# Kernel optimization log

Measured on AMD Instinct MI355X. Metric: run time of the kernel, lower is better.

The kernel has to match this reference:

```python
import jax, jax.numpy as jnp
import numpy as np

HIDDEN = 2048
N_HEADS = 16
N_KV = 8
HEAD_DIM = 128
EPS = 1e-6
THETA = 1000000.0
T = 2048


def _rmsnorm(x, w):
    # x: [T, h, D]; normalize over last dim
    var = jnp.mean(x * x, axis=-1, keepdims=True)
    return x * jax.lax.rsqrt(var + EPS) * w


def _rope(x, positions):
    # neox-style rotate-half, rotary_dim == head_dim
    D = x.shape[-1]
    inv_freq = 1.0 / (THETA ** (jnp.arange(0, D, 2, dtype=jnp.float32) / D))  # [D/2]
    freqs = positions.astype(jnp.float32)[:, None] * inv_freq  # [T, D/2]
    cos = jnp.cos(freqs)[:, None, :]  # [T, 1, D/2]
    sin = jnp.sin(freqs)[:, None, :]
    x1, x2 = jnp.split(x, 2, axis=-1)
    return jnp.concatenate([x1 * cos - x2 * sin, x2 * cos + x1 * sin], axis=-1)


def setup_inputs() -> dict:
    key = jax.random.key(0)
    ks = jax.random.split(key, 7)
    s = 0.02
    return {
        "positions": jnp.arange(T, dtype=jnp.int32),
        "hidden_states": jax.random.normal(ks[0], (T, HIDDEN), dtype=jnp.float32),
        "wq": jax.random.normal(ks[1], (HIDDEN, N_HEADS * HEAD_DIM), dtype=jnp.float32) * s,
        "wk": jax.random.normal(ks[2], (HIDDEN, N_KV * HEAD_DIM), dtype=jnp.float32) * s,
        "wv": jax.random.normal(ks[3], (HIDDEN, N_KV * HEAD_DIM), dtype=jnp.float32) * s,
        "wo": jax.random.normal(ks[4], (N_HEADS * HEAD_DIM, HIDDEN), dtype=jnp.float32) * s,
        "q_norm_w": jnp.ones((HEAD_DIM,), dtype=jnp.float32),
        "k_norm_w": jnp.ones((HEAD_DIM,), dtype=jnp.float32),
    }


def reference(positions, hidden_states, wq, wk, wv, wo, q_norm_w, k_norm_w):
    q = (hidden_states @ wq).reshape(-1, N_HEADS, HEAD_DIM)
    k = (hidden_states @ wk).reshape(-1, N_KV, HEAD_DIM)
    v = (hidden_states @ wv).reshape(-1, N_KV, HEAD_DIM)
    q = _rmsnorm(q, q_norm_w)
    k = _rmsnorm(k, k_norm_w)
    q = _rope(q, positions)
    k = _rope(k, positions)
    # GQA: expand kv heads
    rep = N_HEADS // N_KV
    k = jnp.repeat(k, rep, axis=1)  # [T, H, D]
    v = jnp.repeat(v, rep, axis=1)
    scale = HEAD_DIM ** -0.5
    scores = jnp.einsum('qhd,khd->hqk', q, k) * scale  # [H, T, T]
    tq = q.shape[0]
    causal = jnp.tril(jnp.ones((tq, tq), dtype=bool))
    scores = jnp.where(causal[None], scores, jnp.finfo(scores.dtype).min)
    probs = jax.nn.softmax(scores, axis=-1)
    o = jnp.einsum('hqk,khd->qhd', probs, v).reshape(tq, N_HEADS * HEAD_DIM)
    return o @ wo
```

## Files before the change

### kernel.cpp

```cpp
#include <hip/hip_runtime.h>
#include <cstdint>

#define TT 2048
#define NH 16
#define NKV 8
#define HD 128
#define SCALE_L2E 0.12751743f
#define SM_M2 16.5f

typedef unsigned short u16;
typedef unsigned int u32;
typedef u16 u16x8 __attribute__((ext_vector_type(8)));
typedef __bf16 bf16x8 __attribute__((ext_vector_type(8)));
typedef float f32x4 __attribute__((ext_vector_type(4)));

__device__ inline u16 f2bf(float x){
  u32 u = __builtin_bit_cast(u32, x);
  u = (u + 0x7fffu + ((u >> 16) & 1u)) >> 16;
  return (u16)u;
}
__device__ inline float bf2f(u16 h){
  return __builtin_bit_cast(float, (u32)h << 16);
}
__device__ inline bf16x8 as_bf(u16x8 v){ return __builtin_bit_cast(bf16x8, v); }

__device__ inline void gl_lds16(const void* g, void* l){
  typedef __attribute__((address_space(1))) const void gv_t;
  typedef __attribute__((address_space(3))) void lv_t;
  __builtin_amdgcn_global_load_lds((gv_t*)g, (lv_t*)l, 16, 0, 0);
}

__global__ void cast_f32_bf16(const float* __restrict__ in, u16* __restrict__ out, int n8){
  int i = blockIdx.x * blockDim.x + threadIdx.x;
  if (i < n8){
    const float4* p = (const float4*)(in + (size_t)i * 8);
    float4 a = p[0], b = p[1];
    u16x8 o = { f2bf(a.x), f2bf(a.y), f2bf(a.z), f2bf(a.w),
                f2bf(b.x), f2bf(b.y), f2bf(b.z), f2bf(b.w) };
    *(u16x8*)(out + (size_t)i * 8) = o;
  }
}

__global__ void transpose_cast(const float* __restrict__ in, u16* __restrict__ out, int R, int C){
  __shared__ float tile[32][33];
  int bx = blockIdx.x * 32;
  int by = blockIdx.y * 32;
  int x = threadIdx.x, y = threadIdx.y;
  #pragma unroll
  for (int i = 0; i < 32; i += 8) tile[y + i][x] = in[(size_t)(by + y + i) * C + bx + x];
  __syncthreads();
  #pragma unroll
  for (int i = 0; i < 32; i += 8) out[(size_t)(bx + y + i) * R + by + x] = f2bf(tile[x][y + i]);
}

template<bool F32OUT>
__global__ __launch_bounds__(256, 2) void gemm_bt(const u16* __restrict__ A, const u16* __restrict__ B,
                                                  void* __restrict__ C, int K,
                                                  int lda, int ldb, int ldc){
  __shared__ u16 lds[2][(128 + 128) * 64];
  const int tid = threadIdx.x;
  const int wv = tid >> 6, ln = tid & 63;
  const int lg = ln >> 4, l15 = ln & 15;
  const int m0 = blockIdx.y * 128, n0 = blockIdx.x * 128;
  const int wr = wv >> 1, wc = wv & 1;
  f32x4 acc[4][4] = {};

  auto stage = [&](int buf, int kt){
    const u16* Ab = A + (size_t)m0 * lda + kt * 64;
    const u16* Bb = B + (size_t)n0 * ldb + kt * 64;
    u16* lA = &lds[buf][0];
    u16* lB = &lds[buf][128 * 64];
    #pragma unroll
    for (int it = 0; it < 4; ++it){
      int idx = it * 256 + tid;
      int r = idx >> 3, cs = idx & 7;
      gl_lds16(Ab + (size_t)r * lda + cs * 8, lA + (size_t)(it * 256 + wv * 64) * 8);
    }
    #pragma unroll
    for (int it = 0; it < 4; ++it){
      int idx = it * 256 + tid;
      int r = idx >> 3, cs = idx & 7;
      gl_lds16(Bb + (size_t)r * ldb + cs * 8, lB + (size_t)(it * 256 + wv * 64) * 8);
    }
  };

  stage(0, 0);
  int nk = K / 64;
  for (int kt = 0; kt < nk; ++kt){
    int buf = kt & 1;
    __syncthreads();
    if (kt + 1 < nk) stage(buf ^ 1, kt + 1);
    const u16* lA = &lds[buf][0];
    const u16* lB = &lds[buf][128 * 64];
    #pragma unroll
    for (int kk = 0; kk < 2; ++kk){
      int kof = kk * 32 + lg * 8;
      bf16x8 af[4], bfv[4];
      #pragma unroll
      for (int mm = 0; mm < 4; mm++){
        int row = wr * 64 + mm * 16 + l15;
        af[mm] = as_bf(*(const u16x8*)&lA[row * 64 + kof]);
      }
      #pragma unroll
      for (int nn = 0; nn < 4; nn++){
        int col = wc * 64 + nn * 16 + l15;
        bfv[nn] = as_bf(*(const u16x8*)&lB[col * 64 + kof]);
      }
      #pragma unroll
      for (int mm = 0; mm < 4; mm++)
        #pragma unroll
        for (int nn = 0; nn < 4; nn++)
          acc[mm][nn] = __builtin_amdgcn_mfma_f32_16x16x32_bf16(af[mm], bfv[nn], acc[mm][nn], 0, 0, 0);
    }
  }
  #pragma unroll
  for (int mm = 0; mm < 4; mm++)
    #pragma unroll
    for (int nn = 0; nn < 4; nn++){
      int grow0 = m0 + wr * 64 + mm * 16 + lg * 4;
      int gcol  = n0 + wc * 64 + nn * 16 + l15;
      #pragma unroll
      for (int r = 0; r < 4; r++){
        float v = acc[mm][nn][r];
        if (F32OUT) ((float*)C)[(size_t)(grow0 + r) * ldc + gcol] = v;
        else        ((u16*)C)[(size_t)(grow0 + r) * ldc + gcol] = f2bf(v);
      }
    }
}

__global__ void rmsnorm_rope(const u16* __restrict__ QKV, const int* __restrict__ pos,
                             const float* __restrict__ qw, const float* __restrict__ kw,
                             u16* __restrict__ Qr, u16* __restrict__ Kr){
  int gw = (blockIdx.x * blockDim.x + threadIdx.x) >> 6;
  int ln = threadIdx.x & 63;
  int t = gw / 24, idx = gw % 24;
  if (t >= TT) return;
  bool isq = idx < NH;
  int head = isq ? idx : idx - NH;
  const u16* src = QKV + (size_t)t * 4096 + (isq ? head * HD : 2048 + head * HD);
  const float* wgt = isq ? qw : kw;
  float x0 = bf2f(src[ln]), x1 = bf2f(src[ln + 64]);
  float ss = x0 * x0 + x1 * x1;
  #pragma unroll
  for (int off = 32; off; off >>= 1) ss += __shfl_xor(ss, off);
  float r = rsqrtf(ss * (1.0f / 128.0f) + 1e-6f);
  float xn0 = x0 * r * wgt[ln], xn1 = x1 * r * wgt[ln + 64];
  float inv = exp2f(-(float)ln * 0.311430758895690f);
  float ang = (float)pos[t] * inv;
  float c = cosf(ang), s = sinf(ang);
  float o0 = xn0 * c - xn1 * s;
  float o1 = xn1 * c + xn0 * s;
  u16* dst = isq ? (Qr + (size_t)t * 2048 + head * HD) : (Kr + (size_t)t * 1024 + head * HD);
  dst[ln]      = f2bf(o0);
  dst[ln + 64] = f2bf(o1);
}

__global__ void v_transpose(const u16* __restrict__ QKV, u16* __restrict__ Vt){
  __shared__ u16 tile[64][72];
  int kh = blockIdx.z;
  int d0 = blockIdx.y * 64;
  int t0 = blockIdx.x * 64;
  int tid = threadIdx.x;
  #pragma unroll
  for (int it = 0; it < 2; ++it){
    int idx = it * 256 + tid;
    int tr = idx >> 3, seg = idx & 7;
    *(u16x8*)&tile[tr][seg * 8] =
      *(const u16x8*)(QKV + (size_t)(t0 + tr) * 4096 + 3072 + kh * HD + d0 + seg * 8);
  }
  __syncthreads();
  #pragma unroll
  for (int it = 0; it < 2; ++it){
    int idx = it * 256 + tid;
    int dr = idx >> 3, seg = idx & 7;
    u16x8 v;
    #pragma unroll
    for (int j = 0; j < 8; j++) v[j] = tile[seg * 8 + j][dr];
    *(u16x8*)(Vt + ((size_t)kh * HD + d0 + dr) * 2048 + t0 + seg * 8) = v;
  }
}

__global__ __launch_bounds__(512, 4) void attn(const u16* __restrict__ Qr, const u16* __restrict__ Kr,
                                               const u16* __restrict__ Vt, u16* __restrict__ O){
  extern __shared__ u16 smem[];
  u16* Karea = smem;
  u16* Varea = smem + 16384;
  const int h = blockIdx.y, kh = h >> 1;
  const int qc = (h < 8) ? blockIdx.x : 31 - blockIdx.x;
  const int tid = threadIdx.x, wv = tid >> 6, ln = tid & 63;
  const int i4 = wv & 3, jp = wv >> 2;
  const int lg = ln >> 4, l15 = ln & 15;
  u16* Pw = smem + 32768 + wv * 640;

  auto stage = [&](int buf, int it){
    const int tokl = tid >> 4;
    const int kp = tid & 15;
    const int seg = kp ^ (tokl & 7);
    #pragma unroll
    for (int p = 0; p < 2; ++p){
      int tokg = it * 64 + p * 32 + tokl;
      gl_lds16(Kr + (size_t)tokg * 1024 + kh * HD + seg * 8,
               Karea + (buf * 2 + p) * 4096 + wv * 512);
    }
    const u16* Vb = Vt + (size_t)kh * HD * 2048;
    const int dr = tid >> 2, slot = tid & 3;
    const int tokoff = (slot ^ (dr & 3)) * 8;
    #pragma unroll
    for (int p = 0; p < 2; ++p){
      gl_lds16(Vb + (size_t)dr * 2048 + it * 64 + p * 32 + tokoff,
               Varea + (buf * 2 + p) * 4096 + wv * 512);
    }
  };

  bf16x8 qf[4];
  {
    const u16* qp = Qr + (size_t)(qc * 64 + i4 * 16 + l15) * 2048 + h * HD + lg * 8;
    #pragma unroll
    for (int kk = 0; kk < 4; kk++) qf[kk] = as_bf(*(const u16x8*)(qp + kk * 32));
  }
  const u16x8 ones_u = {0x3f80, 0x3f80, 0x3f80, 0x3f80, 0x3f80, 0x3f80, 0x3f80, 0x3f80};
  const bf16x8 onesf = as_bf(ones_u);

  f32x4 acc[8] = {};
  f32x4 asum = {};

  stage(0, 0);
  const int nit = qc + 1;
  for (int it = 0; it < nit; ++it){
    const int buf = it & 1;
    __syncthreads();
    if (it + 1 < nit) stage(buf ^ 1, it + 1);
    const int t = 2 * it + jp;
    const int D0 = 32 * t - 64 * qc - 16 * i4;
    if (D0 <= 15){
      const u16* Kb = Karea + (buf * 2 + jp) * 4096;
      const u16* Vb2 = Varea + (buf * 2 + jp) * 4096;
      __builtin_amdgcn_s_setprio(1);
      f32x4 c0 = {}, c1 = {};
      if (D0 <= 0){
        #pragma unroll
        for (int kk = 0; kk < 4; ++kk){
          int slot = (kk * 4 + lg) ^ (l15 & 7);
          bf16x8 kf = as_bf(*(const u16x8*)&Kb[l15 * 128 + slot * 8]);
          c0 = __builtin_amdgcn_mfma_f32_16x16x32_bf16(qf[kk], kf, c0, 0, 0, 0);
        }
      }
      if (D0 + 16 <= 0){
        #pragma unroll
        for (int kk = 0; kk < 4; ++kk){
          int tok = 16 + l15;
          int slot = (kk * 4 + lg) ^ (tok & 7);
          bf16x8 kf = as_bf(*(const u16x8*)&Kb[tok * 128 + slot * 8]);
          c1 = __builtin_amdgcn_mfma_f32_16x16x32_bf16(qf[kk], kf, c1, 0, 0, 0);
        }
      }
      __builtin_amdgcn_s_setprio(0);
      #pragma unroll
      for (int s = 0; s < 2; ++s){
        const int D = D0 + 16 * s;
        #pragma unroll
        for (int r = 0; r < 4; ++r){
          int row = lg * 4 + r;
          float pv;
          if (D > 0) pv = 0.f;
          else {
            float x = (s ? c1[r] : c0[r]) * SCALE_L2E - SM_M2;
            if (D == 0 && l15 > row) x = -1e30f;
            pv = exp2f(x);
          }
          Pw[row * 40 + s * 16 + l15] = f2bf(pv);
        }
      }
      bf16x8 pf = as_bf(*(const u16x8*)&Pw[l15 * 40 + lg * 8]);
      __builtin_amdgcn_s_setprio(1);
      asum = __builtin_amdgcn_mfma_f32_16x16x32_bf16(pf, onesf, asum, 0, 0, 0);
      const int vslot = lg ^ (l15 & 3);
      #pragma unroll
      for (int g = 0; g < 8; ++g){
        int d = g * 16 + l15;
        bf16x8 vf = as_bf(*(const u16x8*)&Vb2[d * 32 + vslot * 8]);
        acc[g] = __builtin_amdgcn_mfma_f32_16x16x32_bf16(pf, vf, acc[g], 0, 0, 0);
      }
      __builtin_amdgcn_s_setprio(0);
    }
  }
  __syncthreads();
  float* Ls  = (float*)smem;
  float* LsS = (float*)smem + 8192;
  if (jp == 1){
    #pragma unroll
    for (int g = 0; g < 8; ++g)
      *(f32x4*)&Ls[i4 * 2048 + g * 256 + ln * 4] = acc[g];
    if (l15 == 0){
      #pragma unroll
      for (int r = 0; r < 4; ++r) LsS[i4 * 16 + lg * 4 + r] = asum[r];
    }
  }
  __syncthreads();
  if (jp == 0){
    float rinv[4];
    #pragma unroll
    for (int r = 0; r < 4; ++r)
      rinv[r] = 1.0f / (asum[r] + LsS[i4 * 16 + lg * 4 + r]);
    #pragma unroll
    for (int g = 0; g < 8; ++g){
      f32x4 po = *(const f32x4*)&Ls[i4 * 2048 + g * 256 + ln * 4];
      #pragma unroll
      for (int r = 0; r < 4; ++r){
        float o = (acc[g][r] + po[r]) * rinv[r];
        O[(size_t)(qc * 64 + i4 * 16 + lg * 4 + r) * 2048 + h * HD + g * 16 + l15] = f2bf(o);
      }
    }
  }
}

extern "C" void kernel_launch(void* const* d_in, const int* in_sizes, int n_in,
                              void* d_out, int out_size, void* d_ws, size_t ws_size,
                              hipStream_t stream){
  const int*   positions = (const int*)d_in[0];
  const float* hidden    = (const float*)d_in[1];
  const float* wq        = (const float*)d_in[2];
  const float* wk        = (const float*)d_in[3];
  const float* wv        = (const float*)d_in[4];
  const float* wo        = (const float*)d_in[5];
  const float* qw        = (const float*)d_in[6];
  const float* kw        = (const float*)d_in[7];
  float* out = (float*)d_out;

  char* ws = (char*)d_ws;
  u16* hs   = (u16*)ws; ws += (size_t)2048 * 2048 * 2;
  u16* Wqkv = (u16*)ws; ws += (size_t)4096 * 2048 * 2;
  u16* Wo   = (u16*)ws; ws += (size_t)2048 * 2048 * 2;
  u16* QKV  = (u16*)ws; ws += (size_t)2048 * 4096 * 2;
  u16* Qr   = (u16*)ws; ws += (size_t)2048 * 2048 * 2;
  u16* Kr   = (u16*)ws; ws += (size_t)2048 * 1024 * 2;
  u16* Vt   = (u16*)ws; ws += (size_t)8 * 128 * 2048 * 2;
  u16* O    = (u16*)ws;

  cast_f32_bf16<<<2048, 256, 0, stream>>>(hidden, hs, 2048 * 2048 / 8);
  dim3 tb(32, 8);
  transpose_cast<<<dim3(2048 / 32, 2048 / 32), tb, 0, stream>>>(wq, Wqkv, 2048, 2048);
  transpose_cast<<<dim3(1024 / 32, 2048 / 32), tb, 0, stream>>>(wk, Wqkv + (size_t)2048 * 2048, 2048, 1024);
  transpose_cast<<<dim3(1024 / 32, 2048 / 32), tb, 0, stream>>>(wv, Wqkv + (size_t)3072 * 2048, 2048, 1024);
  transpose_cast<<<dim3(2048 / 32, 2048 / 32), tb, 0, stream>>>(wo, Wo, 2048, 2048);

  gemm_bt<false><<<dim3(4096 / 128, 2048 / 128), 256, 0, stream>>>(hs, Wqkv, QKV, 2048, 2048, 2048, 4096);

  rmsnorm_rope<<<2048 * 24 / 4, 256, 0, stream>>>(QKV, positions, qw, kw, Qr, Kr);
  v_transpose<<<dim3(32, 2, 8), 256, 0, stream>>>(QKV, Vt);

  attn<<<dim3(32, 16), 512, 75776, stream>>>(Qr, Kr, Vt, O);

  gemm_bt<true><<<dim3(2048 / 128, 2048 / 128), 256, 0, stream>>>(O, Wo, out, 2048, 2048, 2048, 2048);
}
```

Before: 161.1 us.

## Rewrite GEMMs with 512-thread 128x256 tiles, triple-buffered swizzled LDS, split-K output

Replaces the 256-thread 128x128 GEMM with a 512-thread kernel that computes 128x256 tiles. Operands are staged through three LDS buffers in about 144 KB of dynamic shared memory, with XOR-swizzled slots, explicit vmcnt waits and raised MFMA priority. This is meant to overlap global loads with compute and reduce LDS bank conflicts. The output projection uses 2-way split-K to get enough blocks. Its two fp32 partial results go into the freed QKV/Qr/Kr/Vt workspace and an extra add kernel sums them, which costs additional memory traffic and one more launch.

```diff
diff --git a/kernel.cpp b/kernel.cpp
--- a/kernel.cpp
+++ b/kernel.cpp
@@ -54,63 +54,77 @@
 }
 
 template<bool F32OUT>
-__global__ __launch_bounds__(256, 2) void gemm_bt(const u16* __restrict__ A, const u16* __restrict__ B,
-                                                  void* __restrict__ C, int K,
-                                                  int lda, int ldb, int ldc){
-  __shared__ u16 lds[2][(128 + 128) * 64];
+__global__ __launch_bounds__(512, 2) void gemm8p(const u16* __restrict__ A, const u16* __restrict__ B,
+                                                 void* __restrict__ Cv, int Klen,
+                                                 int lda, int ldb, int ldc, size_t zstride){
+  extern __shared__ u16 smem[];
   const int tid = threadIdx.x;
   const int wv = tid >> 6, ln = tid & 63;
   const int lg = ln >> 4, l15 = ln & 15;
-  const int m0 = blockIdx.y * 128, n0 = blockIdx.x * 128;
-  const int wr = wv >> 1, wc = wv & 1;
+  const int wr = wv >> 2, wc = wv & 3;
+  const int m0 = blockIdx.y * 128, n0 = blockIdx.x * 256;
+  const int Kofs = blockIdx.z * Klen;
+  const u16* Ab0 = A + (size_t)m0 * lda + Kofs;
+  const u16* Bb0 = B + (size_t)n0 * ldb + Kofs;
   f32x4 acc[4][4] = {};
 
-  auto stage = [&](int buf, int kt){
-    const u16* Ab = A + (size_t)m0 * lda + kt * 64;
-    const u16* Bb = B + (size_t)n0 * ldb + kt * 64;
-    u16* lA = &lds[buf][0];
-    u16* lB = &lds[buf][128 * 64];
+  auto stage = [&](int sbuf, int kt){
+    u16* base = smem + sbuf * 24576;
+    const u16* Ak = Ab0 + kt * 64;
+    #pragma unroll
+    for (int it = 0; it < 2; ++it){
+      int idx = it * 512 + tid;
+      int r = idx >> 3, sl = idx & 7, g = sl ^ (r & 7);
+      gl_lds16(Ak + (size_t)r * lda + g * 8, base + (it * 512 + wv * 64) * 8);
+    }
+    const u16* Bk = Bb0 + kt * 64;
+    u16* bbase = base + 8192;
     #pragma unroll
     for (int it = 0; it < 4; ++it){
-      int idx = it * 256 + tid;
-      int r = idx >> 3, cs = idx & 7;
-      gl_lds16(Ab + (size_t)r * lda + cs * 8, lA + (size_t)(it * 256 + wv * 64) * 8);
-    }
-    #pragma unroll
-    for (int it = 0; it < 4; ++it){
-      int idx = it * 256 + tid;
-      int r = idx >> 3, cs = idx & 7;
-      gl_lds16(Bb + (size_t)r * ldb + cs * 8, lB + (size_t)(it * 256 + wv * 64) * 8);
+      int idx = it * 512 + tid;
+      int r = idx >> 3, sl = idx & 7, g = sl ^ (r & 7);
+      gl_lds16(Bk + (size_t)r * ldb + g * 8, bbase + (it * 512 + wv * 64) * 8);
     }
   };
 
+  const int nk = Klen / 64;
   stage(0, 0);
-  int nk = K / 64;
+  if (nk > 1) stage(1, 1);
   for (int kt = 0; kt < nk; ++kt){
-    int buf = kt & 1;
-    __syncthreads();
-    if (kt + 1 < nk) stage(buf ^ 1, kt + 1);
-    const u16* lA = &lds[buf][0];
-    const u16* lB = &lds[buf][128 * 64];
+    if (kt + 2 < nk){
+      stage((kt + 2) % 3, kt + 2);
+      asm volatile("s_waitcnt vmcnt(12)" ::: "memory");
+    } else if (kt + 1 < nk){
+      asm volatile("s_waitcnt vmcnt(6)" ::: "memory");
+    } else {
+      asm volatile("s_waitcnt vmcnt(0)" ::: "memory");
+    }
+    __builtin_amdgcn_s_barrier();
+    const u16* lA = smem + (kt % 3) * 24576;
+    const u16* lB = lA + 8192;
     #pragma unroll
     for (int kk = 0; kk < 2; ++kk){
-      int kof = kk * 32 + lg * 8;
       bf16x8 af[4], bfv[4];
       #pragma unroll
       for (int mm = 0; mm < 4; mm++){
-        int row = wr * 64 + mm * 16 + l15;
-        af[mm] = as_bf(*(const u16x8*)&lA[row * 64 + kof]);
+        int ra = wr * 64 + mm * 16 + l15;
+        int slot = (kk * 4 + lg) ^ (ra & 7);
+        af[mm] = as_bf(*(const u16x8*)&lA[(ra * 8 + slot) * 8]);
       }
       #pragma unroll
       for (int nn = 0; nn < 4; nn++){
-        int col = wc * 64 + nn * 16 + l15;
-        bfv[nn] = as_bf(*(const u16x8*)&lB[col * 64 + kof]);
-      }
+        int cb = wc * 64 + nn * 16 + l15;
+        int slot = (kk * 4 + lg) ^ (cb & 7);
+        bfv[nn] = as_bf(*(const u16x8*)&lB[(cb * 8 + slot) * 8]);
+      }
+      __builtin_amdgcn_s_setprio(1);
       #pragma unroll
       for (int mm = 0; mm < 4; mm++)
         #pragma unroll
         for (int nn = 0; nn < 4; nn++)
           acc[mm][nn] = __builtin_amdgcn_mfma_f32_16x16x32_bf16(af[mm], bfv[nn], acc[mm][nn], 0, 0, 0);
+      __builtin_amdgcn_s_setprio(0);
+      __builtin_amdgcn_s_barrier();
     }
   }
   #pragma unroll
@@ -122,10 +136,20 @@
       #pragma unroll
       for (int r = 0; r < 4; r++){
         float v = acc[mm][nn][r];
-        if (F32OUT) ((float*)C)[(size_t)(grow0 + r) * ldc + gcol] = v;
-        else        ((u16*)C)[(size_t)(grow0 + r) * ldc + gcol] = f2bf(v);
-      }
-    }
+        if (F32OUT) ((float*)Cv + blockIdx.z * zstride)[(size_t)(grow0 + r) * ldc + gcol] = v;
+        else        ((u16*)Cv)[(size_t)(grow0 + r) * ldc + gcol] = f2bf(v);
+      }
+    }
+}
+
+__global__ void add_f32(const float* __restrict__ a, const float* __restrict__ b,
+                        float* __restrict__ o, int n4){
+  int i = blockIdx.x * blockDim.x + threadIdx.x;
+  if (i < n4){
+    float4 x = ((const float4*)a)[i], y = ((const float4*)b)[i];
+    float4 z = { x.x + y.x, x.y + y.y, x.z + y.z, x.w + y.w };
+    ((float4*)o)[i] = z;
+  }
 }
 
 __global__ void rmsnorm_rope(const u16* __restrict__ QKV, const int* __restrict__ pos,
@@ -344,12 +368,15 @@
   transpose_cast<<<dim3(1024 / 32, 2048 / 32), tb, 0, stream>>>(wv, Wqkv + (size_t)3072 * 2048, 2048, 1024);
   transpose_cast<<<dim3(2048 / 32, 2048 / 32), tb, 0, stream>>>(wo, Wo, 2048, 2048);
 
-  gemm_bt<false><<<dim3(4096 / 128, 2048 / 128), 256, 0, stream>>>(hs, Wqkv, QKV, 2048, 2048, 2048, 4096);
+  gemm8p<false><<<dim3(16, 16, 1), 512, 147456, stream>>>(hs, Wqkv, QKV, 2048, 2048, 2048, 4096, 0);
 
   rmsnorm_rope<<<2048 * 24 / 4, 256, 0, stream>>>(QKV, positions, qw, kw, Qr, Kr);
   v_transpose<<<dim3(32, 2, 8), 256, 0, stream>>>(QKV, Vt);
 
   attn<<<dim3(32, 16), 512, 75776, stream>>>(Qr, Kr, Vt, O);
 
-  gemm_bt<true><<<dim3(2048 / 128, 2048 / 128), 256, 0, stream>>>(O, Wo, out, 2048, 2048, 2048, 2048);
-}
+  float* p0 = (float*)QKV;
+  gemm8p<true><<<dim3(8, 16, 2), 512, 147456, stream>>>(O, Wo, p0, 1024, 2048, 2048, 2048,
+                                                        (size_t)2048 * 2048);
+  add_f32<<<4096, 256, 0, stream>>>(p0, p0 + (size_t)2048 * 2048, out, 2048 * 2048 / 4);
+}
```

Measured after the change: 159.9 us. About the same (-0.7%).
